# Kernel tuning notes

Measured on AMD Instinct MI355X. Metric: run time of the kernel, lower is better.

## Reference

```python
import jax, jax.numpy as jnp
import numpy as np
import math

N_BATCH = 65536
T_STEPS = 512
BETA_INIT = 0.9  # beta_ stored as logit of beta
THRESH_INIT = 1.0


def setup_inputs() -> dict:
    key = jax.random.key(0)
    k_x, k_u = jax.random.split(key)
    x = jax.random.normal(k_x, (N_BATCH, T_STEPS), dtype=jnp.float32)
    beta_ = jnp.array([math.log(BETA_INIT / (1.0 - BETA_INIT))], dtype=jnp.float32)
    threshold = jnp.array([THRESH_INIT], dtype=jnp.float32)
    init_u = jax.random.uniform(k_u, (N_BATCH,), dtype=jnp.float32)  # torch.rand(N)
    return {"x": x, "beta_": beta_, "threshold": threshold, "init_u": init_u}


def _lif_scan(x, beta_, threshold, init_u):
    sg = jax.lax.stop_gradient
    beta = jax.nn.sigmoid(beta_)  # [1]
    thr = threshold               # [1]
    mem0 = init_u * sg(thr)       # random_state init: rand(N)*threshold.detach() -> [N]

    def step(mem, x_t):
        mem_in = mem                              # memory entering this step (logged)
        mem_upd = beta * mem + x_t                # StateUpdate
        surplus = mem_upd - thr
        hard = (surplus >= 0).astype(mem_upd.dtype)
        soft = jax.nn.sigmoid(surplus)
        spike = sg(hard) + soft - sg(soft)        # straight-through surrogate
        mem_post = mem_upd - sg(hard) * sg(thr)   # StatePostupdate (detached reset)
        return mem_post, (spike, mem_in)

    _, (spikes, mems) = jax.lax.scan(step, mem0, jnp.swapaxes(x, 0, 1))  # over T
    # memories list in torch = [init, m1..m_{T-1}] i.e. memory BEFORE each step
    return jnp.swapaxes(spikes, 0, 1), jnp.swapaxes(mems, 0, 1)  # each [N, T]


def reference(x, beta_, threshold, init_u):
    return _lif_scan(x, beta_, threshold, init_u)
```

## Files before the change

kernel.cpp:

```cpp
#include <hip/hip_runtime.h>
#include <math.h>


constexpr int N_BATCH = 65536;
constexpr int T_STEPS = 512;
constexpr int BLOCK   = 64;
constexpr int ROWS    = 64;
constexpr int TILE    = 32;
constexpr int NCH     = T_STEPS / TILE;
constexpr int PAD     = TILE + 1;

__global__ __launch_bounds__(BLOCK) void lif_scan_kernel(
    const float* __restrict__ x,
    const float* __restrict__ beta_p,
    const float* __restrict__ thr_p,
    const float* __restrict__ init_u,
    float* __restrict__ out)
{
#pragma clang fp contract(off)
    __shared__ float xs [ROWS * PAD];
    __shared__ float ssb[ROWS * PAD];
    __shared__ float msb[ROWS * PAD];

    const int t    = threadIdx.x;
    const int base = blockIdx.x * ROWS;
    const int rsub = t >> 3;
    const int a    = t & 7;

    const float thr  = thr_p[0];
    const float beta = (float)(1.0 / (1.0 + exp(-(double)beta_p[0])));
    float mem = __fmul_rn(init_u[base + t], thr);

    const float4* __restrict__ xg = (const float4*)x;
    float4* __restrict__ sg = (float4*)out;
    float4* __restrict__ mg = (float4*)(out + (size_t)N_BATCH * T_STEPS);

    float4 v[8];
#pragma unroll
    for (int p = 0; p < 8; ++p)
        v[p] = xg[(size_t)(base + p * 8 + rsub) * 128 + a];

    for (int c = 0; c < NCH; ++c) {
#pragma unroll
        for (int p = 0; p < 8; ++p) {
            const int r = p * 8 + rsub;
            float* dst = &xs[r * PAD + a * 4];
            dst[0] = v[p].x; dst[1] = v[p].y; dst[2] = v[p].z; dst[3] = v[p].w;
        }
        if (c + 1 < NCH) {
#pragma unroll
            for (int p = 0; p < 8; ++p)
                v[p] = xg[(size_t)(base + p * 8 + rsub) * 128 + (c + 1) * 8 + a];
        }
#pragma unroll
        for (int k = 0; k < TILE; ++k) {
            const float xv      = xs[t * PAD + k];
            const float mem_in  = mem;
            const float mem_upd = __fadd_rn(__fmul_rn(beta, mem), xv);
            const float surplus = __fsub_rn(mem_upd, thr);
            const float hard    = (surplus >= 0.0f) ? 1.0f : 0.0f;
            ssb[t * PAD + k] = hard;
            msb[t * PAD + k] = mem_in;
            mem = __fsub_rn(mem_upd, __fmul_rn(hard, thr));
        }
#pragma unroll
        for (int p = 0; p < 8; ++p) {
            const int r = p * 8 + rsub;
            const float* srow = &ssb[r * PAD + a * 4];
            const float* mrow = &msb[r * PAD + a * 4];
            const float4 sv = make_float4(srow[0], srow[1], srow[2], srow[3]);
            const float4 mv = make_float4(mrow[0], mrow[1], mrow[2], mrow[3]);
            const size_t gi = (size_t)(base + r) * 128 + (size_t)c * 8 + a;
            sg[gi] = sv;
            mg[gi] = mv;
        }
    }
}

extern "C" void kernel_launch(void* const* d_in, const int* in_sizes, int n_in,
                              void* d_out, int out_size, void* d_ws, size_t ws_size,
                              hipStream_t stream) {
    const float* x      = (const float*)d_in[0];
    const float* beta_  = (const float*)d_in[1];
    const float* thresh = (const float*)d_in[2];
    const float* init_u = (const float*)d_in[3];
    float* out = (float*)d_out;

    dim3 block(BLOCK);
    dim3 grid(N_BATCH / ROWS);
    lif_scan_kernel<<<grid, block, 0, stream>>>(x, beta_, thresh, init_u, out);
}
```

Before: 370.5 us.

## Double-buffer 64-step tiles with nontemporal loads/stores and in-place spike staging

Doubles the time tile to 64 steps and keeps two chunks of input in flight in registers (va/vb), prefetching two chunks ahead so global loads overlap the serial scan. Spikes are written back into the input LDS tile instead of a separate buffer, which cuts LDS use, and global loads and stores use nontemporal hints. The cost is much higher register pressure (32 float4 prefetch registers), with launch_bounds(64,1) allowing the compiler to use them. With only 64-thread blocks, occupancy may be limited.

```diff
diff --git a/kernel.cpp b/kernel.cpp
--- a/kernel.cpp
+++ b/kernel.cpp
@@ -1,16 +1,53 @@
 #include <hip/hip_runtime.h>
 #include <math.h>
 
+
+typedef float f32x4 __attribute__((ext_vector_type(4)));
 
 constexpr int N_BATCH = 65536;
 constexpr int T_STEPS = 512;
 constexpr int BLOCK   = 64;
 constexpr int ROWS    = 64;
-constexpr int TILE    = 32;
+constexpr int TILE    = 64;
 constexpr int NCH     = T_STEPS / TILE;
 constexpr int PAD     = TILE + 1;
+constexpr int RPF     = T_STEPS / 4;
 
-__global__ __launch_bounds__(BLOCK) void lif_scan_kernel(
+
+__device__ __forceinline__ void prefetch_chunk(f32x4 (&v)[16], const f32x4* __restrict__ xg,
+                                               int base, int rsub, int a, int c) {
+#pragma unroll
+    for (int p = 0; p < 16; ++p)
+        v[p] = __builtin_nontemporal_load(
+            &xg[(size_t)(base + p * 4 + rsub) * RPF + (size_t)c * 16 + a]);
+}
+
+__device__ __forceinline__ void stage_chunk(const f32x4 (&v)[16], float* xs, int rsub, int a) {
+#pragma unroll
+    for (int p = 0; p < 16; ++p) {
+        const int r = p * 4 + rsub;
+        float* dst = &xs[r * PAD + a * 4];
+        dst[0] = v[p][0]; dst[1] = v[p][1]; dst[2] = v[p][2]; dst[3] = v[p][3];
+    }
+}
+
+__device__ __forceinline__ void store_chunk(const float* xs, const float* msb,
+                                            f32x4* __restrict__ sg, f32x4* __restrict__ mg,
+                                            int base, int rsub, int a, int c) {
+#pragma unroll
+    for (int p = 0; p < 16; ++p) {
+        const int r = p * 4 + rsub;
+        const float* srow = &xs [r * PAD + a * 4];
+        const float* mrow = &msb[r * PAD + a * 4];
+        const f32x4 sv = { srow[0], srow[1], srow[2], srow[3] };
+        const f32x4 mv = { mrow[0], mrow[1], mrow[2], mrow[3] };
+        const size_t gi = (size_t)(base + r) * RPF + (size_t)c * 16 + a;
+        __builtin_nontemporal_store(sv, &sg[gi]);
+        __builtin_nontemporal_store(mv, &mg[gi]);
+    }
+}
+
+__global__ __launch_bounds__(BLOCK, 1) void lif_scan_kernel(
     const float* __restrict__ x,
     const float* __restrict__ beta_p,
     const float* __restrict__ thr_p,
@@ -19,39 +56,27 @@
 {
 #pragma clang fp contract(off)
     __shared__ float xs [ROWS * PAD];
-    __shared__ float ssb[ROWS * PAD];
     __shared__ float msb[ROWS * PAD];
 
     const int t    = threadIdx.x;
     const int base = blockIdx.x * ROWS;
-    const int rsub = t >> 3;
-    const int a    = t & 7;
+    const int rsub = t >> 4;
+    const int a    = t & 15;
 
     const float thr  = thr_p[0];
     const float beta = (float)(1.0 / (1.0 + exp(-(double)beta_p[0])));
     float mem = __fmul_rn(init_u[base + t], thr);
 
-    const float4* __restrict__ xg = (const float4*)x;
-    float4* __restrict__ sg = (float4*)out;
-    float4* __restrict__ mg = (float4*)(out + (size_t)N_BATCH * T_STEPS);
+    const f32x4* __restrict__ xg = (const f32x4*)x;
+    f32x4* __restrict__ sg = (f32x4*)out;
+    f32x4* __restrict__ mg = (f32x4*)(out + (size_t)N_BATCH * T_STEPS);
 
-    float4 v[8];
-#pragma unroll
-    for (int p = 0; p < 8; ++p)
-        v[p] = xg[(size_t)(base + p * 8 + rsub) * 128 + a];
+    f32x4 va[16], vb[16];
+    prefetch_chunk(va, xg, base, rsub, a, 0);
+    prefetch_chunk(vb, xg, base, rsub, a, 1);
 
-    for (int c = 0; c < NCH; ++c) {
-#pragma unroll
-        for (int p = 0; p < 8; ++p) {
-            const int r = p * 8 + rsub;
-            float* dst = &xs[r * PAD + a * 4];
-            dst[0] = v[p].x; dst[1] = v[p].y; dst[2] = v[p].z; dst[3] = v[p].w;
-        }
-        if (c + 1 < NCH) {
-#pragma unroll
-            for (int p = 0; p < 8; ++p)
-                v[p] = xg[(size_t)(base + p * 8 + rsub) * 128 + (c + 1) * 8 + a];
-        }
+    auto compute_chunk = [&]() {
+#pragma clang fp contract(off)
 #pragma unroll
         for (int k = 0; k < TILE; ++k) {
             const float xv      = xs[t * PAD + k];
@@ -59,21 +84,22 @@
             const float mem_upd = __fadd_rn(__fmul_rn(beta, mem), xv);
             const float surplus = __fsub_rn(mem_upd, thr);
             const float hard    = (surplus >= 0.0f) ? 1.0f : 0.0f;
-            ssb[t * PAD + k] = hard;
+            xs [t * PAD + k] = hard;
             msb[t * PAD + k] = mem_in;
             mem = __fsub_rn(mem_upd, __fmul_rn(hard, thr));
         }
-#pragma unroll
-        for (int p = 0; p < 8; ++p) {
-            const int r = p * 8 + rsub;
-            const float* srow = &ssb[r * PAD + a * 4];
-            const float* mrow = &msb[r * PAD + a * 4];
-            const float4 sv = make_float4(srow[0], srow[1], srow[2], srow[3]);
-            const float4 mv = make_float4(mrow[0], mrow[1], mrow[2], mrow[3]);
-            const size_t gi = (size_t)(base + r) * 128 + (size_t)c * 8 + a;
-            sg[gi] = sv;
-            mg[gi] = mv;
-        }
+    };
+
+    for (int c = 0; c < NCH; c += 2) {
+        stage_chunk(va, xs, rsub, a);
+        if (c + 2 < NCH) prefetch_chunk(va, xg, base, rsub, a, c + 2);
+        compute_chunk();
+        store_chunk(xs, msb, sg, mg, base, rsub, a, c);
+
+        stage_chunk(vb, xs, rsub, a);
+        if (c + 3 < NCH) prefetch_chunk(vb, xg, base, rsub, a, c + 3);
+        compute_chunk();
+        store_chunk(xs, msb, sg, mg, base, rsub, a, c + 1);
     }
 }
 
```

Result: faster. 363.0 us (-2.0%).
